# Optimization experiments

Measured on AMD Instinct MI355X. Metric: run time of the kernel, lower is better.

The kernel has to match this reference:

```python
import jax, jax.numpy as jnp
import numpy as np

GRID = 24          # sqrt(576)
MM = 1024          # mm_hidden_size
HID = 4096         # hidden_size
HEADS = 8          # mm_hidden_size // 128
NQ = GRID * GRID   # 576 queries / tokens
BATCH = 16
K = 2              # top-k == num_experts == 2


def _sincos_1d(d, pos):
    omega = np.arange(d // 2, dtype=np.float32) / (d / 2.0)
    omega = 1.0 / 10000 ** omega
    out = np.einsum('m,d->md', pos.reshape(-1).astype(np.float32), omega)
    return np.concatenate([np.sin(out), np.cos(out)], axis=1)


def _sincos_2d(d, g):
    gw, gh = np.meshgrid(np.arange(g, dtype=np.float32), np.arange(g, dtype=np.float32))
    return np.concatenate([_sincos_1d(d // 2, gh), _sincos_1d(d // 2, gw)], axis=1)


def layer_norm(x, g, b, eps=1e-5):
    mu = x.mean(-1, keepdims=True)
    var = ((x - mu) ** 2).mean(-1, keepdims=True)
    return (x - mu) * jax.lax.rsqrt(var + eps) * g + b


def mha(q, k, v, Wi, bi, Wo, bo, H):
    # q,k,v: [N, S, D]; Wi: [3D, D]; torch nn.MultiheadAttention semantics
    N, S, D = q.shape
    dh = D // H
    Wq, Wk, Wv = Wi[:D], Wi[D:2 * D], Wi[2 * D:]
    bq, bk, bv = bi[:D], bi[D:2 * D], bi[2 * D:]
    qp = (q @ Wq.T + bq).reshape(N, S, H, dh)
    kp = (k @ Wk.T + bk).reshape(N, -1, H, dh)
    vp = (v @ Wv.T + bv).reshape(N, -1, H, dh)
    scale = jnp.asarray(1.0 / np.sqrt(dh), q.dtype)
    scores = jnp.einsum('bqhd,bkhd->bhqk', qp, kp) * scale
    attn = jax.nn.softmax(scores, axis=-1)
    out = jnp.einsum('bhqk,bkhd->bqhd', attn, vp).reshape(N, S, D)
    return out @ Wo.T + bo


def _gating(xf, w_gate, w_noise, noise):
    # noisy top-k gating, training mode, k == num_experts == 2
    clean = xf @ w_gate                               # [B, 2]
    std = jax.nn.softplus(xf @ w_noise) + 0.01
    logits = jax.nn.softmax(clean + noise * std, axis=1)
    top_vals, top_idx = jax.lax.top_k(logits, K)      # min(k+1, n) == 2
    gates_k = top_vals / (top_vals.sum(1, keepdims=True) + 1e-6)
    rows = jnp.arange(xf.shape[0])[:, None]
    return jnp.zeros_like(logits).at[rows, top_idx].set(gates_k)


def setup_inputs() -> dict:
    key = jax.random.key(0)
    ks = jax.random.split(key, 10)
    s = 0.02
    f32 = jnp.float32
    return dict(
        x=jax.random.normal(ks[0], (BATCH, NQ, MM), f32),
        noise=jax.random.normal(ks[1], (BATCH * NQ, 2), f32),
        W1=jax.random.normal(ks[2], (HID, MM), f32) * s,
        b1=jnp.zeros((HID,), f32),
        W2=jax.random.normal(ks[3], (HID, HID), f32) * s,
        b2=jnp.zeros((HID,), f32),
        query=jax.random.normal(ks[4], (NQ, MM), f32) * s,
        pos_embed=jnp.asarray(_sincos_2d(MM, GRID), f32),
        ln_q_g=jnp.ones((MM,), f32), ln_q_b=jnp.zeros((MM,), f32),
        ln_kv_g=jnp.ones((MM,), f32), ln_kv_b=jnp.zeros((MM,), f32),
        in_proj_w=jax.random.normal(ks[5], (3 * MM, MM), f32) * s,
        in_proj_b=jnp.zeros((3 * MM,), f32),
        out_w=jax.random.normal(ks[6], (MM, MM), f32) * s,
        out_b=jnp.zeros((MM,), f32),
        w_gate=jax.random.normal(ks[7], (MM, 2), f32) * s,
        w_noise=jax.random.normal(ks[8], (MM, 2), f32) * s,
    )


def reference(x, noise, W1, b1, W2, b2, query, pos_embed, ln_q_g, ln_q_b,
              ln_kv_g, ln_kv_b, in_proj_w, in_proj_b, out_w, out_b,
              w_gate, w_noise):
    N, C, D = x.shape

    def projection(t):  # Linear -> GELU(exact) -> Linear
        h = jax.nn.gelu(t @ W1.T + b1, approximate=False)
        return h @ W2.T + b2

    # --- Resampler expert (kv_proj/ln_post/proj are identity here) ---
    kv = layer_norm(x, ln_kv_g, ln_kv_b)                    # [N, 576, D]
    q = layer_norm(query, ln_q_g, ln_q_b) + pos_embed       # [576, D]
    q = jnp.broadcast_to(q, (N, C, D))
    attn_out = mha(q, kv + pos_embed, kv, in_proj_w, in_proj_b, out_w, out_b, HEADS)

    e0 = projection(x)          # expert 0: MLP projection
    e1 = projection(attn_out)   # expert 1: resampler then projection

    gates = _gating(x.reshape(N * C, D), w_gate, w_noise, noise).reshape(N, C, 2)
    # stack(...,-1) @ gates[...,None] squeezed == gated sum over experts
    return e0 * gates[..., 0:1] + e1 * gates[..., 1:2]
```

## Files before the change

### kernel.cpp

```cpp
#include <hip/hip_runtime.h>
#include <hip/hip_bf16.h>
#include <cstdint>
#include <cstddef>


typedef __bf16 bf16;
typedef __bf16 bf16x4 __attribute__((ext_vector_type(4)));
typedef __bf16 bf16x8 __attribute__((ext_vector_type(8)));
typedef float  f32x4  __attribute__((ext_vector_type(4)));

#define BATCH 16
#define NQ    576
#define MM    1024
#define HID   4096
#define HEADS 8
#define DH    128
#define ROWS  (BATCH*NQ)

typedef const unsigned int __attribute__((address_space(1)))* gas_ptr;
typedef unsigned int __attribute__((address_space(3)))* las_ptr;

__device__ __forceinline__ void async16(const bf16* g, bf16* l) {
  __builtin_amdgcn_global_load_lds((gas_ptr)g, (las_ptr)l, 16, 0, 0);
}

__global__ __launch_bounds__(256) void cvt_kernel(
    const float* __restrict__ s, bf16* __restrict__ d)
{
  const int i = (blockIdx.x * 256 + threadIdx.x) * 4;
  f32x4 v = *(const f32x4*)(s + i);
  bf16x4 o;
#pragma unroll
  for (int j = 0; j < 4; ++j) o[j] = (bf16)v[j];
  *(bf16x4*)(d + i) = o;
}

enum { MODE_BIAS = 0, MODE_GG = 1, MODE_GGACC = 2, MODE_GB = 3 };

template <int MODE, typename OutT>
__global__ __launch_bounds__(256) void gemm_bt(
    const bf16* __restrict__ A, const bf16* __restrict__ W,
    const float* __restrict__ bias, OutT* __restrict__ C,
    const float* __restrict__ gates, int M, int N, int K)
{
  __shared__ bf16 As[128 * 64];
  __shared__ bf16 Bs[128 * 64];

  const int tid  = threadIdx.x;
  const int lane = tid & 63;
  const int w    = tid >> 6;
  const int wm   = (w & 1) * 64;
  const int wn   = (w >> 1) * 64;
  const int l15  = lane & 15;
  const int quad = lane >> 4;
  const int m0   = blockIdx.y * 128;
  const int n0   = blockIdx.x * 128;

  f32x4 acc[4][4] = {};

  const int srow0  = tid >> 3;
  const int schunk = (tid & 7) ^ (srow0 & 7);
  int arows[4], brows[4];
#pragma unroll
  for (int j = 0; j < 4; ++j) {
    int r = m0 + j * 32 + srow0; if (r > M - 1) r = M - 1;
    arows[j] = r;
    brows[j] = n0 + j * 32 + srow0;
  }
  const int kc = schunk * 8;
  bf16* lA = As + tid * 8;
  bf16* lB = Bs + tid * 8;

  const int axb  = (quad ^ (l15 & 7)) * 8;
  const int axb1 = axb ^ 32;

  for (int kt = 0; kt < K; kt += 64) {
#pragma unroll
    for (int j = 0; j < 4; ++j)
      async16(A + (size_t)arows[j] * K + kt + kc, lA + j * 2048);
#pragma unroll
    for (int j = 0; j < 4; ++j)
      async16(W + (size_t)brows[j] * K + kt + kc, lB + j * 2048);
    __syncthreads();

    bf16x8 af[4], bfr[4];
#pragma unroll
    for (int i = 0; i < 4; ++i)
      af[i] = *(const bf16x8*)(As + (wm + i * 16 + l15) * 64 + axb);
#pragma unroll
    for (int i = 0; i < 4; ++i)
      bfr[i] = *(const bf16x8*)(Bs + (wn + i * 16 + l15) * 64 + axb);
#pragma unroll
    for (int mi = 0; mi < 4; ++mi)
#pragma unroll
      for (int ni = 0; ni < 4; ++ni)
        acc[mi][ni] = __builtin_amdgcn_mfma_f32_16x16x32_bf16(
            af[mi], bfr[ni], acc[mi][ni], 0, 0, 0);
#pragma unroll
    for (int i = 0; i < 4; ++i)
      af[i] = *(const bf16x8*)(As + (wm + i * 16 + l15) * 64 + axb1);
#pragma unroll
    for (int i = 0; i < 4; ++i)
      bfr[i] = *(const bf16x8*)(Bs + (wn + i * 16 + l15) * 64 + axb1);
#pragma unroll
    for (int mi = 0; mi < 4; ++mi)
#pragma unroll
      for (int ni = 0; ni < 4; ++ni)
        acc[mi][ni] = __builtin_amdgcn_mfma_f32_16x16x32_bf16(
            af[mi], bfr[ni], acc[mi][ni], 0, 0, 0);
    __syncthreads();
  }

#pragma unroll
  for (int ni = 0; ni < 4; ++ni) {
    const int col = n0 + wn + ni * 16 + l15;
    const float bv = bias[col];
#pragma unroll
    for (int mi = 0; mi < 4; ++mi) {
      const int rowb = m0 + wm + mi * 16 + quad * 4;
#pragma unroll
      for (int r = 0; r < 4; ++r) {
        const int gr = rowb + r;
        if (gr < M) {
          const size_t idx = (size_t)gr * N + col;
          if (MODE == MODE_GB) {
            C[idx] = (OutT)(acc[mi][ni][r] +
                            (gates[gr * 2] + gates[gr * 2 + 1]) * bv);
          } else {
            float v = acc[mi][ni][r] + bv;
            if (MODE == MODE_GG || MODE == MODE_GGACC)
              v = 0.5f * v * (1.0f + erff(v * 0.70710678118654752f));
            if (MODE == MODE_GG)
              C[idx] = (OutT)(v * gates[gr * 2]);
            else if (MODE == MODE_GGACC)
              C[idx] = (OutT)((float)C[idx] + v * gates[gr * 2 + 1]);
            else
              C[idx] = (OutT)v;
          }
        }
      }
    }
  }
}

__global__ __launch_bounds__(256) void attn_kernel(
    const bf16* __restrict__ qp, const bf16* __restrict__ kp,
    const bf16* __restrict__ vp, bf16* __restrict__ ctx)
{
  __shared__ bf16 Qs[64 * 128];
  __shared__ bf16 Ks[64 * 128];
  __shared__ bf16 Vt[128 * 64];
  __shared__ bf16 Ps[64 * 64];

  const int qt = blockIdx.x, b = blockIdx.y, h = blockIdx.z;
  const int tid = threadIdx.x, lane = tid & 63, w = tid >> 6;
  const int l15 = lane & 15, quad = lane >> 4;
  const int q0 = qt * 64;

#pragma unroll
  for (int i = 0; i < 4; ++i) {
    const int c = i * 256 + tid;
    const int row = c >> 4, col = (c & 15) * 8;
    *(bf16x8*)(Qs + row * 128 + col) =
        *(const bf16x8*)(qp + (size_t)(q0 + row) * MM + h * DH + col);
  }

  float m_r[4], l_r[4];
  f32x4 accO[8] = {};
#pragma unroll
  for (int r = 0; r < 4; ++r) { m_r[r] = -1e30f; l_r[r] = 0.f; }

  const float scale = 0.08838834764831843f;

  for (int kt = 0; kt < 9; ++kt) {
    __syncthreads();
    const int kbase = b * NQ + kt * 64;
#pragma unroll
    for (int i = 0; i < 4; ++i) {
      const int c = i * 256 + tid;
      const int row = c >> 4, col = (c & 15) * 8;
      *(bf16x8*)(Ks + row * 128 + col) =
          *(const bf16x8*)(kp + (size_t)(kbase + row) * MM + h * DH + col);
      bf16x8 vv = *(const bf16x8*)(vp + (size_t)(kbase + row) * MM + h * DH + col);
#pragma unroll
      for (int j = 0; j < 8; ++j) Vt[(col + j) * 64 + row] = vv[j];
    }
    __syncthreads();

    f32x4 sacc[4] = {};
#pragma unroll
    for (int kcq = 0; kcq < 4; ++kcq) {
      bf16x8 aq = *(const bf16x8*)(Qs + (w * 16 + l15) * 128 + kcq * 32 + quad * 8);
#pragma unroll
      for (int ni = 0; ni < 4; ++ni) {
        bf16x8 bk = *(const bf16x8*)(Ks + (ni * 16 + l15) * 128 + kcq * 32 + quad * 8);
        sacc[ni] = __builtin_amdgcn_mfma_f32_16x16x32_bf16(aq, bk, sacc[ni], 0, 0, 0);
      }
    }
#pragma unroll
    for (int ni = 0; ni < 4; ++ni)
#pragma unroll
      for (int r = 0; r < 4; ++r) sacc[ni][r] *= scale;

    float p[4][4];
#pragma unroll
    for (int r = 0; r < 4; ++r) {
      float mx = fmaxf(fmaxf(sacc[0][r], sacc[1][r]), fmaxf(sacc[2][r], sacc[3][r]));
#pragma unroll
      for (int off = 8; off >= 1; off >>= 1) mx = fmaxf(mx, __shfl_xor(mx, off, 64));
      const float mnew = fmaxf(m_r[r], mx);
      const float al = expf(m_r[r] - mnew);
      float rs = 0.f;
#pragma unroll
      for (int ni = 0; ni < 4; ++ni) { p[ni][r] = expf(sacc[ni][r] - mnew); rs += p[ni][r]; }
#pragma unroll
      for (int off = 8; off >= 1; off >>= 1) rs += __shfl_xor(rs, off, 64);
      l_r[r] = l_r[r] * al + rs;
      m_r[r] = mnew;
#pragma unroll
      for (int ni2 = 0; ni2 < 8; ++ni2) accO[ni2][r] *= al;
    }

#pragma unroll
    for (int ni = 0; ni < 4; ++ni)
#pragma unroll
      for (int r = 0; r < 4; ++r)
        Ps[(w * 16 + quad * 4 + r) * 64 + ni * 16 + l15] = (bf16)p[ni][r];

#pragma unroll
    for (int kc2 = 0; kc2 < 2; ++kc2) {
      bf16x8 ap = *(const bf16x8*)(Ps + (w * 16 + l15) * 64 + kc2 * 32 + quad * 8);
#pragma unroll
      for (int ni2 = 0; ni2 < 8; ++ni2) {
        bf16x8 bv = *(const bf16x8*)(Vt + (ni2 * 16 + l15) * 64 + kc2 * 32 + quad * 8);
        accO[ni2] = __builtin_amdgcn_mfma_f32_16x16x32_bf16(ap, bv, accO[ni2], 0, 0, 0);
      }
    }
  }

#pragma unroll
  for (int r = 0; r < 4; ++r) {
    const float inv = 1.0f / l_r[r];
    const int qrow = q0 + w * 16 + quad * 4 + r;
#pragma unroll
    for (int ni2 = 0; ni2 < 8; ++ni2)
      ctx[(size_t)(b * NQ + qrow) * MM + h * DH + ni2 * 16 + l15] =
          (bf16)(accO[ni2][r] * inv);
  }
}

__global__ __launch_bounds__(256) void lnx_kernel(
    const float* __restrict__ x, const float* __restrict__ g,
    const float* __restrict__ bta, const float* __restrict__ pos,
    const float* __restrict__ wg, const float* __restrict__ wn,
    const float* __restrict__ noise,
    bf16* __restrict__ kv, bf16* __restrict__ kin,
    bf16* __restrict__ x_bf, float* __restrict__ gates)
{
  const int row = blockIdx.x, tid = threadIdx.x;
  f32x4 xv = *(const f32x4*)(x + (size_t)row * MM + tid * 4);

  float s = 0.f, ss = 0.f, a0 = 0.f, a1 = 0.f, c0 = 0.f, c1 = 0.f;
#pragma unroll
  for (int j = 0; j < 4; ++j) {
    const int c = tid * 4 + j;
    s  += xv[j];
    ss += xv[j] * xv[j];
    a0 += xv[j] * wg[c * 2];
    a1 += xv[j] * wg[c * 2 + 1];
    c0 += xv[j] * wn[c * 2];
    c1 += xv[j] * wn[c * 2 + 1];
  }

  {
    bf16x4 o;
#pragma unroll
    for (int j = 0; j < 4; ++j) o[j] = (bf16)xv[j];
    *(bf16x4*)(x_bf + (size_t)row * MM + tid * 4) = o;
  }

#pragma unroll
  for (int off = 32; off >= 1; off >>= 1) {
    s  += __shfl_xor(s,  off, 64);  ss += __shfl_xor(ss, off, 64);
    a0 += __shfl_xor(a0, off, 64);  a1 += __shfl_xor(a1, off, 64);
    c0 += __shfl_xor(c0, off, 64);  c1 += __shfl_xor(c1, off, 64);
  }
  __shared__ float red[24];
  const int w = tid >> 6;
  if ((tid & 63) == 0) {
    red[w * 6]     = s;  red[w * 6 + 1] = ss;
    red[w * 6 + 2] = a0; red[w * 6 + 3] = a1;
    red[w * 6 + 4] = c0; red[w * 6 + 5] = c1;
  }
  __syncthreads();
  s  = red[0] + red[6]  + red[12] + red[18];
  ss = red[1] + red[7]  + red[13] + red[19];

  const float mu   = s * (1.0f / MM);
  const float rsig = rsqrtf(ss * (1.0f / MM) - mu * mu + 1e-5f);
  const int prow = row % NQ;
#pragma unroll
  for (int j = 0; j < 4; ++j) {
    const int c = tid * 4 + j;
    const float y = (xv[j] - mu) * rsig * g[c] + bta[c];
    kv[(size_t)row * MM + c]  = (bf16)y;
    kin[(size_t)row * MM + c] = (bf16)(y + pos[(size_t)prow * MM + c]);
  }

  if (tid == 0) {
    a0 = red[2] + red[8]  + red[14] + red[20];
    a1 = red[3] + red[9]  + red[15] + red[21];
    c0 = red[4] + red[10] + red[16] + red[22];
    c1 = red[5] + red[11] + red[17] + red[23];
    const float sp0 = fmaxf(c0, 0.f) + log1pf(expf(-fabsf(c0)));
    const float sp1 = fmaxf(c1, 0.f) + log1pf(expf(-fabsf(c1)));
    const float l0 = a0 + noise[row * 2]     * (sp0 + 0.01f);
    const float l1 = a1 + noise[row * 2 + 1] * (sp1 + 0.01f);
    const float mx = fmaxf(l0, l1);
    const float e0 = expf(l0 - mx), e1 = expf(l1 - mx);
    const float inv = 1.0f / (e0 + e1);
    const float p0 = e0 * inv, p1 = e1 * inv;
    const float den = 1.0f / (p0 + p1 + 1e-6f);
    gates[row * 2]     = p0 * den;
    gates[row * 2 + 1] = p1 * den;
  }
}

__global__ __launch_bounds__(256) void ln_q_kernel(
    const float* __restrict__ query, const float* __restrict__ g,
    const float* __restrict__ bta, const float* __restrict__ pos,
    bf16* __restrict__ qout)
{
  const int row = blockIdx.x, tid = threadIdx.x;
  f32x4 xv = *(const f32x4*)(query + (size_t)row * MM + tid * 4);
  float s = 0.f, ss = 0.f;
#pragma unroll
  for (int j = 0; j < 4; ++j) { s += xv[j]; ss += xv[j] * xv[j]; }
#pragma unroll
  for (int off = 32; off >= 1; off >>= 1) { s += __shfl_xor(s, off, 64); ss += __shfl_xor(ss, off, 64); }
  __shared__ float red[8];
  const int w = tid >> 6;
  if ((tid & 63) == 0) { red[w] = s; red[4 + w] = ss; }
  __syncthreads();
  s  = red[0] + red[1] + red[2] + red[3];
  ss = red[4] + red[5] + red[6] + red[7];
  const float mu = s * (1.0f / MM);
  const float rsig = rsqrtf(ss * (1.0f / MM) - mu * mu + 1e-5f);
#pragma unroll
  for (int j = 0; j < 4; ++j) {
    const int c = tid * 4 + j;
    const float y = (xv[j] - mu) * rsig * g[c] + bta[c] + pos[(size_t)row * MM + c];
    qout[(size_t)row * MM + c] = (bf16)y;
  }
}

extern "C" void kernel_launch(void* const* d_in, const int* in_sizes, int n_in,
                              void* d_out, int out_size, void* d_ws, size_t ws_size,
                              hipStream_t stream)
{
  const float* x       = (const float*)d_in[0];
  const float* noise   = (const float*)d_in[1];
  const float* W1      = (const float*)d_in[2];
  const float* b1      = (const float*)d_in[3];
  const float* W2      = (const float*)d_in[4];
  const float* b2      = (const float*)d_in[5];
  const float* query   = (const float*)d_in[6];
  const float* pos     = (const float*)d_in[7];
  const float* ln_q_g  = (const float*)d_in[8];
  const float* ln_q_b  = (const float*)d_in[9];
  const float* ln_kv_g = (const float*)d_in[10];
  const float* ln_kv_b = (const float*)d_in[11];
  const float* ipw     = (const float*)d_in[12];
  const float* ipb     = (const float*)d_in[13];
  const float* out_w   = (const float*)d_in[14];
  const float* out_b   = (const float*)d_in[15];
  const float* w_gate  = (const float*)d_in[16];
  const float* w_noise = (const float*)d_in[17];
  float* out = (float*)d_out;

  char* ws = (char*)d_ws;
  bf16*  kin   = (bf16*)(ws);
  bf16*  ctx   = kin;
  bf16*  kp    = (bf16*)(ws + 18874368);
  bf16*  vp    = (bf16*)(ws + 37748736);
  bf16*  qbuf  = (bf16*)(ws + 56623104);
  bf16*  qp    = (bf16*)(ws + 57802752);
  bf16*  ipwb  = (bf16*)(ws + 58982400);
  bf16*  outwb = (bf16*)(ws + 65273856);
  bf16*  h     = (bf16*)(ws);
  bf16*  x_bf  = (bf16*)(ws + 75497472);
  bf16*  W1b   = (bf16*)(ws + 94371840);
  bf16*  W2b   = (bf16*)(ws + 102760448);
  float* gates = (float*)(ws + 136314880);
  bf16*  kv       = (bf16*)d_out;
  bf16*  attn_out = (bf16*)((char*)d_out + 18874368);

  cvt_kernel<<<4096,  256, 0, stream>>>(W1, W1b);
  cvt_kernel<<<16384, 256, 0, stream>>>(W2, W2b);
  cvt_kernel<<<3072,  256, 0, stream>>>(ipw,   ipwb);
  cvt_kernel<<<1024,  256, 0, stream>>>(out_w, outwb);
  lnx_kernel<<<ROWS, 256, 0, stream>>>(x, ln_kv_g, ln_kv_b, pos,
                                       w_gate, w_noise, noise,
                                       kv, kin, x_bf, gates);
  ln_q_kernel<<<NQ, 256, 0, stream>>>(query, ln_q_g, ln_q_b, pos, qbuf);

  gemm_bt<MODE_BIAS, bf16><<<dim3(8, 5),  256, 0, stream>>>(qbuf, ipwb, ipb, qp, nullptr, NQ, MM, MM);
  gemm_bt<MODE_BIAS, bf16><<<dim3(8, 72), 256, 0, stream>>>(kin, ipwb + (size_t)MM * MM, ipb + MM, kp, nullptr, ROWS, MM, MM);
  gemm_bt<MODE_BIAS, bf16><<<dim3(8, 72), 256, 0, stream>>>(kv, ipwb + (size_t)2 * MM * MM, ipb + 2 * MM, vp, nullptr, ROWS, MM, MM);

  attn_kernel<<<dim3(9, BATCH, HEADS), 256, 0, stream>>>(qp, kp, vp, ctx);

  gemm_bt<MODE_BIAS, bf16><<<dim3(8, 72), 256, 0, stream>>>(ctx, outwb, out_b, attn_out, nullptr, ROWS, MM, MM);

  gemm_bt<MODE_GG,    bf16><<<dim3(32, 72), 256, 0, stream>>>(x_bf,     W1b, b1, h, gates, ROWS, HID, MM);
  gemm_bt<MODE_GGACC, bf16><<<dim3(32, 72), 256, 0, stream>>>(attn_out, W1b, b1, h, gates, ROWS, HID, MM);
  gemm_bt<MODE_GB,   float><<<dim3(32, 72), 256, 0, stream>>>(h,        W2b, b2, out, gates, ROWS, HID, HID);
}
```

Baseline: 1.335 ms.

## Add 256x256-tile pipelined GEMM for the large MLP projections

Adds a new 512-thread GEMM kernel with 256x256 output tiles, double-buffered LDS filled by async global-to-LDS loads with XOR swizzle, and four MFMA phases per K-step that interleave prefetches with compute under raised wave priority. The three large projection GEMMs (W1 twice and W2) now use it instead of the 128x128 kernel. The larger tile raises arithmetic intensity and cuts global/L2 traffic, at the cost of 128KB of LDS, heavy register use, and fewer blocks (576), which can leave CUs unevenly loaded.

```diff
diff --git a/kernel.cpp b/kernel.cpp
--- a/kernel.cpp
+++ b/kernel.cpp
@@ -36,6 +36,165 @@
 }
 
 enum { MODE_BIAS = 0, MODE_GG = 1, MODE_GGACC = 2, MODE_GB = 3 };
+
+template <int MODE, typename OutT>
+__global__ __launch_bounds__(512, 2) void gemm_256(
+    const bf16* __restrict__ A, const bf16* __restrict__ W,
+    const float* __restrict__ bias, OutT* __restrict__ C,
+    const float* __restrict__ gates, int M, int N, int K)
+{
+  __shared__ bf16 LDS[2 * 32768];
+
+  const int tid  = threadIdx.x;
+  const int lane = tid & 63;
+  const int w    = tid >> 6;
+  const int w_m  = w >> 2;
+  const int w_n  = w & 3;
+  const int l15  = lane & 15;
+  const int quad = lane >> 4;
+  const int m0   = blockIdx.y * 256;
+  const int n0   = blockIdx.x * 256;
+
+  auto stA = [&](int buf, int rowOff, int kt) {
+    const int r = rowOff + (tid >> 3);
+    async16(A + (size_t)(m0 + r) * K + kt + (((tid & 7) ^ (r & 7)) << 3),
+            LDS + buf * 32768 + r * 64 + ((tid & 7) << 3));
+  };
+  auto stB = [&](int buf, int rowOff, int kt) {
+    const int r = rowOff + (tid >> 3);
+    async16(W + (size_t)(n0 + r) * K + kt + (((tid & 7) ^ (r & 7)) << 3),
+            LDS + buf * 32768 + 16384 + r * 64 + ((tid & 7) << 3));
+  };
+
+  const int aoff0 = ((0 + quad) ^ (l15 & 7)) * 8;
+  const int aoff1 = ((4 + quad) ^ (l15 & 7)) * 8;
+  const int arow  = w_m * 128 + l15;
+  const int brow  = w_n * 64 + l15;
+
+  f32x4 acc[8][4] = {};
+  const int nt = K >> 6;
+
+  stB(0, 0, 0);   stB(0, 64, 0);  stB(0, 128, 0); stB(0, 192, 0);
+  stA(0, 0, 0);   stA(0, 64, 0);  stA(0, 128, 0); stA(0, 192, 0);
+  stB(1, 0, 64);  stB(1, 64, 64); stB(1, 128, 64); stB(1, 192, 64);
+  stA(1, 0, 64);  stA(1, 128, 64);
+  asm volatile("s_waitcnt vmcnt(6)" ::: "memory");
+  __builtin_amdgcn_sched_barrier(0);
+  __builtin_amdgcn_s_barrier();
+
+  for (int t = 0; t < nt; ++t) {
+    const int cb = t & 1;
+    const int nb = cb ^ 1;
+    const bf16* Ab = LDS + cb * 32768;
+    const bf16* Bb = Ab + 16384;
+    const bool pf1 = (t + 1 < nt);
+    const bool pf2 = (t + 2 < nt);
+    const int kt1 = (t + 1) << 6;
+    const int kt2 = (t + 2) << 6;
+
+    bf16x8 bfr[4][2];
+    bf16x8 af0, af1, af2, af3;
+
+#define READ_A(MB)                                                         \
+    af0 = *(const bf16x8*)(Ab + ((MB) * 16 + arow) * 64 + aoff0);          \
+    af1 = *(const bf16x8*)(Ab + ((MB) * 16 + arow) * 64 + aoff1);          \
+    af2 = *(const bf16x8*)(Ab + ((MB) * 16 + 16 + arow) * 64 + aoff0);     \
+    af3 = *(const bf16x8*)(Ab + ((MB) * 16 + 16 + arow) * 64 + aoff1);
+
+#define DO_MFMA(MB)                                                        \
+    _Pragma("unroll")                                                      \
+    for (int ni = 0; ni < 4; ++ni) {                                       \
+      acc[MB][ni]     = __builtin_amdgcn_mfma_f32_16x16x32_bf16(           \
+          af0, bfr[ni][0], acc[MB][ni], 0, 0, 0);                          \
+      acc[MB][ni]     = __builtin_amdgcn_mfma_f32_16x16x32_bf16(           \
+          af1, bfr[ni][1], acc[MB][ni], 0, 0, 0);                          \
+      acc[MB + 1][ni] = __builtin_amdgcn_mfma_f32_16x16x32_bf16(           \
+          af2, bfr[ni][0], acc[MB + 1][ni], 0, 0, 0);                      \
+      acc[MB + 1][ni] = __builtin_amdgcn_mfma_f32_16x16x32_bf16(           \
+          af3, bfr[ni][1], acc[MB + 1][ni], 0, 0, 0);                      \
+    }
+
+#define PHASE_SYNC                                                         \
+    __builtin_amdgcn_s_barrier();                                          \
+    asm volatile("s_waitcnt lgkmcnt(0)" ::: "memory");                     \
+    __builtin_amdgcn_sched_barrier(0);
+
+#pragma unroll
+    for (int ni = 0; ni < 4; ++ni) {
+      bfr[ni][0] = *(const bf16x8*)(Bb + (brow + ni * 16) * 64 + aoff0);
+      bfr[ni][1] = *(const bf16x8*)(Bb + (brow + ni * 16) * 64 + aoff1);
+    }
+    READ_A(0)
+    if (pf1) { stA(nb, 64, kt1); stA(nb, 192, kt1); }
+    PHASE_SYNC
+    __builtin_amdgcn_s_setprio(1);
+    DO_MFMA(0)
+    __builtin_amdgcn_s_setprio(0);
+    __builtin_amdgcn_s_barrier();
+
+    READ_A(2)
+    if (pf2) { stB(cb, 0, kt2); stB(cb, 64, kt2); }
+    PHASE_SYNC
+    __builtin_amdgcn_s_setprio(1);
+    DO_MFMA(2)
+    __builtin_amdgcn_s_setprio(0);
+    __builtin_amdgcn_s_barrier();
+
+    READ_A(4)
+    if (pf2) { stB(cb, 128, kt2); stB(cb, 192, kt2); }
+    PHASE_SYNC
+    __builtin_amdgcn_s_setprio(1);
+    DO_MFMA(4)
+    __builtin_amdgcn_s_setprio(0);
+    __builtin_amdgcn_s_barrier();
+
+    READ_A(6)
+    if (pf2) { stA(cb, 0, kt2); stA(cb, 128, kt2); }
+    if (pf1) {
+      if (pf2) { asm volatile("s_waitcnt vmcnt(6)" ::: "memory"); }
+      else     { asm volatile("s_waitcnt vmcnt(0)" ::: "memory"); }
+      __builtin_amdgcn_sched_barrier(0);
+    }
+    PHASE_SYNC
+    __builtin_amdgcn_s_setprio(1);
+    DO_MFMA(6)
+    __builtin_amdgcn_s_setprio(0);
+    __builtin_amdgcn_s_barrier();
+
+#undef READ_A
+#undef DO_MFMA
+#undef PHASE_SYNC
+  }
+
+#pragma unroll
+  for (int ni = 0; ni < 4; ++ni) {
+    const int col = n0 + w_n * 64 + ni * 16 + l15;
+    const float bv = bias[col];
+#pragma unroll
+    for (int mi = 0; mi < 8; ++mi) {
+      const int rowb = m0 + w_m * 128 + mi * 16 + quad * 4;
+#pragma unroll
+      for (int r = 0; r < 4; ++r) {
+        const int gr = rowb + r;
+        const size_t idx = (size_t)gr * N + col;
+        if (MODE == MODE_GB) {
+          C[idx] = (OutT)(acc[mi][ni][r] +
+                          (gates[gr * 2] + gates[gr * 2 + 1]) * bv);
+        } else {
+          float v = acc[mi][ni][r] + bv;
+          if (MODE == MODE_GG || MODE == MODE_GGACC)
+            v = 0.5f * v * (1.0f + erff(v * 0.70710678118654752f));
+          if (MODE == MODE_GG)
+            C[idx] = (OutT)(v * gates[gr * 2]);
+          else if (MODE == MODE_GGACC)
+            C[idx] = (OutT)((float)C[idx] + v * gates[gr * 2 + 1]);
+          else
+            C[idx] = (OutT)v;
+        }
+      }
+    }
+  }
+}
 
 template <int MODE, typename OutT>
 __global__ __launch_bounds__(256) void gemm_bt(
@@ -412,7 +571,7 @@
 
   gemm_bt<MODE_BIAS, bf16><<<dim3(8, 72), 256, 0, stream>>>(ctx, outwb, out_b, attn_out, nullptr, ROWS, MM, MM);
 
-  gemm_bt<MODE_GG,    bf16><<<dim3(32, 72), 256, 0, stream>>>(x_bf,     W1b, b1, h, gates, ROWS, HID, MM);
-  gemm_bt<MODE_GGACC, bf16><<<dim3(32, 72), 256, 0, stream>>>(attn_out, W1b, b1, h, gates, ROWS, HID, MM);
-  gemm_bt<MODE_GB,   float><<<dim3(32, 72), 256, 0, stream>>>(h,        W2b, b2, out, gates, ROWS, HID, HID);
-}
+  gemm_256<MODE_GG,    bf16><<<dim3(16, 36), 512, 0, stream>>>(x_bf,     W1b, b1, h, gates, ROWS, HID, MM);
+  gemm_256<MODE_GGACC, bf16><<<dim3(16, 36), 512, 0, stream>>>(attn_out, W1b, b1, h, gates, ROWS, HID, MM);
+  gemm_256<MODE_GB,   float><<<dim3(16, 36), 512, 0, stream>>>(h,        W2b, b2, out, gates, ROWS, HID, HID);
+}
```

After: 1.380 ms. 1.03x slower.
